# Performance work log

Hardware: AMD Instinct MI355X
Metric: run time of the kernel (lower is better)

Reference implementation:

```python
import jax, jax.numpy as jnp
import numpy as np

TEMPERATURE = 0.1  # init kwarg
EPS = 1e-8        # torch cosine_similarity eps


def setup_inputs() -> dict:
    key = jax.random.key(0)
    k1, k2, k3 = jax.random.split(key, 3)
    B, D, C = 4096, 1024, 32
    representations = jax.random.normal(k1, (B, D), dtype=jnp.float32)
    soft_labels = jax.random.uniform(k2, (B, C), dtype=jnp.float32)
    labels = jax.random.randint(k3, (B,), 0, 32, dtype=jnp.int64)
    return {
        "representations": representations,
        "soft_labels": soft_labels,
        "labels": labels,
        "pseudo_weight": 10,
    }


def reference(representations, soft_labels, labels, pseudo_weight):
    B = representations.shape[0]
    # row-normalize (cosine similarity)
    norms = jnp.maximum(jnp.linalg.norm(representations, axis=1, keepdims=True), EPS)
    rn = representations / norms
    Z = (rn @ rn.T) / TEMPERATURE                      # [B, B] scaled cosine sims
    E = jnp.exp(Z)
    off_diag = 1.0 - jnp.eye(B, dtype=Z.dtype)         # exclude j == i
    denom = jnp.sum(E * off_diag, axis=1, keepdims=True)   # [B, 1]
    loss_arr = -(Z - jnp.log(denom))                   # -log(exp(Z_ij)/denom_i)
    # positive-pair weights: same label, j != i (detached in original)
    pos = (labels[:, None] == labels[None, :]).astype(Z.dtype) * off_diag
    soft_sim = jax.lax.stop_gradient(soft_labels @ soft_labels.T)  # torch.inner, detached
    w = pos + pseudo_weight * soft_sim
    return jnp.sum(loss_arr * w) / B
```

## Files before the change

kernel.cpp:

```cpp
#include <hip/hip_runtime.h>
#include <hip/hip_bf16.h>
#include <stdint.h>


typedef float f32x4 __attribute__((ext_vector_type(4)));
typedef long i64;

#define INV_T 10.0f
#define Z_SCALE (INV_T / 256.0f)

#define GLD16(gp, lp)                                                          \
    __builtin_amdgcn_global_load_lds(                                          \
        (const __attribute__((address_space(1))) uint32_t*)(gp),               \
        (__attribute__((address_space(3))) uint32_t*)(lp), 16, 0, 0)

#define OFF_RNF8  0
#define OFF_DENOM 4194304
#define OFF_POSS  (OFF_DENOM + 16384)
#define OFF_G     (OFF_POSS + 16384)
#define OFF_CSUM  (OFF_G + 131072)
#define OFF_CCNT  (OFF_CSUM + 128)
#define OFF_OACC  (OFF_CCNT + 128)
#define OFF_DONE  (OFF_OACC + 16)
#define WS_END    (OFF_DONE + 16)
#define ZERO_BYTES (WS_END - OFF_DENOM)

__global__ __launch_bounds__(256) void scl_norm_prep(const float* __restrict__ rep,
                                                     const float* __restrict__ sl,
                                                     const int* __restrict__ labels,
                                                     uint32_t* __restrict__ rnf8,
                                                     float* __restrict__ csum,
                                                     int* __restrict__ ccnt) {
    int b = blockIdx.x;
    int t = threadIdx.x;
    if (b < 4096) {
        int row = b;
        const float4* src = reinterpret_cast<const float4*>(rep + (size_t)row * 1024);
        float4 v = src[t];
        float s = v.x * v.x + v.y * v.y + v.z * v.z + v.w * v.w;
#pragma unroll
        for (int m = 1; m < 64; m <<= 1) s += __shfl_xor(s, m, 64);
        __shared__ float red[4];
        if ((t & 63) == 0) red[t >> 6] = s;
        __syncthreads();
        s = red[0] + red[1] + red[2] + red[3];
        float nf = 16.0f / fmaxf(sqrtf(s), 1e-8f);
        int p = 0;
        p = __builtin_amdgcn_cvt_pk_fp8_f32(v.x * nf, v.y * nf, p, false);
        p = __builtin_amdgcn_cvt_pk_fp8_f32(v.z * nf, v.w * nf, p, true);
        rnf8[row * 256 + t] = (uint32_t)p;
    } else {
        __shared__ float part[8][32];
        __shared__ int bins[32];
        int bb = b - 4096;
        if (t < 32) bins[t] = 0;
        __syncthreads();
        if (t < 128) atomicAdd(&bins[labels[bb * 128 + t]], 1);
        int c = t & 31, rg = t >> 5;
        float s = 0.f;
#pragma unroll 4
        for (int k = 0; k < 16; ++k) {
            int i = bb * 128 + rg * 16 + k;
            s += sl[i * 32 + c];
        }
        part[rg][c] = s;
        __syncthreads();
        if (t < 32) {
            float tot = 0.f;
#pragma unroll
            for (int g = 0; g < 8; ++g) tot += part[g][t];
            atomicAdd(&csum[t], tot);
            atomicAdd(&ccnt[t], bins[t]);
        }
    }
}

__global__ __launch_bounds__(256) void scl_G(const uint8_t* __restrict__ rnf8,
                                             const float* __restrict__ sl,
                                             float* __restrict__ G) {
    int t = threadIdx.x;
    int dblk = blockIdx.x & 15, ks = blockIdx.x >> 4;
    int dq = t >> 5, c = t & 31;
    int d0 = dblk * 64 + dq * 8;
    float acc[8];
#pragma unroll
    for (int j = 0; j < 8; ++j) acc[j] = 0.f;
    int i0 = ks * 128;
#pragma unroll 4
    for (int k = 0; k < 128; ++k) {
        int i = i0 + k;
        uint2 rv = *(const uint2*)&rnf8[(size_t)i * 1024 + d0];
        float sv = sl[i * 32 + c];
        acc[0] += __builtin_amdgcn_cvt_f32_fp8((int)rv.x, 0) * sv;
        acc[1] += __builtin_amdgcn_cvt_f32_fp8((int)rv.x, 1) * sv;
        acc[2] += __builtin_amdgcn_cvt_f32_fp8((int)rv.x, 2) * sv;
        acc[3] += __builtin_amdgcn_cvt_f32_fp8((int)rv.x, 3) * sv;
        acc[4] += __builtin_amdgcn_cvt_f32_fp8((int)rv.y, 0) * sv;
        acc[5] += __builtin_amdgcn_cvt_f32_fp8((int)rv.y, 1) * sv;
        acc[6] += __builtin_amdgcn_cvt_f32_fp8((int)rv.y, 2) * sv;
        acc[7] += __builtin_amdgcn_cvt_f32_fp8((int)rv.y, 3) * sv;
    }
#pragma unroll
    for (int j = 0; j < 8; ++j)
        atomicAdd(&G[(d0 + j) * 32 + c], acc[j] * 0.0625f);
}

__global__ __launch_bounds__(256) void scl_gemm(const uint8_t* __restrict__ rnf8,
                                                const int* __restrict__ labels,
                                                float* __restrict__ denom,
                                                float* __restrict__ posS) {
    __shared__ __align__(16) uint8_t As[128 * 64];
    __shared__ __align__(16) uint8_t Bs[128 * 64];
    __shared__ int lblA[128], lblB[128];

    int L = blockIdx.x;
    int bi = 0, rem = L;
    while (rem >= 32 - bi) { rem -= 32 - bi; ++bi; }
    int bj = bi + rem;
    int rowA0 = bi * 128, colB0 = bj * 128;

    int tid = threadIdx.x;
    if (tid < 128) {
        lblA[tid] = labels[rowA0 + tid];
        lblB[tid] = labels[colB0 + tid];
    }

    int lane = tid & 63, warp = tid >> 6;
    int wr = warp >> 1, wc = warp & 1;
    int m_ = lane & 15, g = lane >> 4;

    int r4 = lane >> 2;
    int csw = (lane & 3) ^ ((lane >> 3) & 3);
    const uint8_t* gA0 = rnf8 + (size_t)(rowA0 + warp * 32 + r4) * 1024 + csw * 16;
    const uint8_t* gB0 = rnf8 + (size_t)(colB0 + warp * 32 + r4) * 1024 + csw * 16;

    f32x4 acc[4][4];
#pragma unroll
    for (int a = 0; a < 4; ++a)
#pragma unroll
        for (int b = 0; b < 4; ++b) acc[a][b] = (f32x4){0.f, 0.f, 0.f, 0.f};

    for (int kt = 0; kt < 16; ++kt) {
        __syncthreads();
        GLD16(gA0 + kt * 64,          &As[(warp * 32) * 64]);
        GLD16(gA0 + kt * 64 + 16384,  &As[(warp * 32 + 16) * 64]);
        GLD16(gB0 + kt * 64,          &Bs[(warp * 32) * 64]);
        GLD16(gB0 + kt * 64 + 16384,  &Bs[(warp * 32 + 16) * 64]);
        __syncthreads();
#pragma unroll
        for (int s = 0; s < 2; ++s) {
            i64 af[4], bf[4];
#pragma unroll
            for (int ti = 0; ti < 4; ++ti) {
                int rowLoc = wr * 64 + ti * 16 + m_;
                af[ti] = *(const i64*)&As[rowLoc * 64 + (((s * 4 + g) ^ (m_ & 6)) * 8)];
            }
#pragma unroll
            for (int tj = 0; tj < 4; ++tj) {
                int colLoc = wc * 64 + tj * 16 + m_;
                bf[tj] = *(const i64*)&Bs[colLoc * 64 + (((s * 4 + g) ^ (m_ & 6)) * 8)];
            }
#pragma unroll
            for (int ti = 0; ti < 4; ++ti)
#pragma unroll
                for (int tj = 0; tj < 4; ++tj)
                    acc[ti][tj] = __builtin_amdgcn_mfma_f32_16x16x32_fp8_fp8(
                        af[ti], bf[tj], acc[ti][tj], 0, 0, 0);
        }
    }

    bool isDiag = (bi == bj);
    int cl = m_;
    float colE[4] = {0.f, 0.f, 0.f, 0.f}, colP[4] = {0.f, 0.f, 0.f, 0.f};
#pragma unroll
    for (int ti = 0; ti < 4; ++ti) {
        int rowLoc = wr * 64 + ti * 16 + g * 4;
        float rE[4] = {0.f, 0.f, 0.f, 0.f}, rP[4] = {0.f, 0.f, 0.f, 0.f};
        int lr[4];
#pragma unroll
        for (int r = 0; r < 4; ++r) lr[r] = lblA[rowLoc + r];
#pragma unroll
        for (int tj = 0; tj < 4; ++tj) {
            int colLoc = wc * 64 + tj * 16 + cl;
            int gCol = colB0 + colLoc;
            int lc = lblB[colLoc];
            f32x4 a = acc[ti][tj];
#pragma unroll
            for (int r = 0; r < 4; ++r) {
                int gRow = rowA0 + rowLoc + r;
                float z = Z_SCALE * a[r];
                float e = __expf(z);
                bool offd = (gRow != gCol);
                if (!offd) e = 0.f;
                rE[r] += e;
                colE[tj] += e;
                if (offd && (lr[r] == lc)) { rP[r] += z; colP[tj] += z; }
            }
        }
#pragma unroll
        for (int r = 0; r < 4; ++r) {
            float v = rE[r], p = rP[r];
#pragma unroll
            for (int msk = 1; msk < 16; msk <<= 1) {
                v += __shfl_xor(v, msk, 64);
                p += __shfl_xor(p, msk, 64);
            }
            if (cl == 0) {
                int gRow = rowA0 + rowLoc + r;
                atomicAdd(&denom[gRow], v);
                atomicAdd(&posS[gRow], p);
            }
        }
    }
    if (!isDiag) {
#pragma unroll
        for (int tj = 0; tj < 4; ++tj) {
            float v = colE[tj], p = colP[tj];
            v += __shfl_xor(v, 16, 64); p += __shfl_xor(p, 16, 64);
            v += __shfl_xor(v, 32, 64); p += __shfl_xor(p, 32, 64);
            if (g == 0) {
                int gCol = colB0 + wc * 64 + tj * 16 + cl;
                atomicAdd(&denom[gCol], v);
                atomicAdd(&posS[gCol], p);
            }
        }
    }
}

__global__ __launch_bounds__(256) void scl_finalize(const float* __restrict__ denom,
                                                    const float* __restrict__ posS,
                                                    const float* __restrict__ sl,
                                                    const int* __restrict__ labels,
                                                    const int* __restrict__ ccnt,
                                                    const float* __restrict__ csum,
                                                    const float* __restrict__ G,
                                                    const int* __restrict__ pwp,
                                                    double* __restrict__ oacc,
                                                    int* __restrict__ done,
                                                    float* __restrict__ out) {
    int t = threadIdx.x;
    int bits = *pwp;
    float pw = (bits >= -(1 << 22) && bits <= (1 << 22)) ? (float)bits : __int_as_float(bits);
    __shared__ double wsum[4];
    double contrib = 0.0;

    if (blockIdx.x < 16) {
        int i = blockIdx.x * 256 + t;
        const f32x4* sl4 = (const f32x4*)sl;
        const f32x4* cs4 = (const f32x4*)csum;
        float dW = 0.f;
#pragma unroll
        for (int q = 0; q < 8; ++q) {
            f32x4 s = sl4[i * 8 + q];
            f32x4 c = cs4[q];
            dW += s[0] * c[0] + s[1] * c[1] + s[2] * c[2] + s[3] * c[3];
        }
        float W = (float)(ccnt[labels[i]] - 1) + pw * dW;
        float term = __logf(denom[i]) * W - posS[i];
        double td = (double)term;
#pragma unroll
        for (int m = 1; m < 64; m <<= 1) td += __shfl_xor(td, m, 64);
        if ((t & 63) == 0) wsum[t >> 6] = td;
        __syncthreads();
        contrib = wsum[0] + wsum[1] + wsum[2] + wsum[3];
    } else {
        const f32x4* G4 = (const f32x4*)G;
        float gs = 0.f;
#pragma unroll
        for (int q = 0; q < 32; ++q) {
            f32x4 v = G4[q * 256 + t];
            gs += v[0] * v[0] + v[1] * v[1] + v[2] * v[2] + v[3] * v[3];
        }
        double gd = (double)gs;
#pragma unroll
        for (int m = 1; m < 64; m <<= 1) gd += __shfl_xor(gd, m, 64);
        if ((t & 63) == 0) wsum[t >> 6] = gd;
        __syncthreads();
        contrib = -(double)(pw * INV_T) * (wsum[0] + wsum[1] + wsum[2] + wsum[3]);
    }

    if (t == 0) {
        atomicAdd(oacc, contrib);
        __threadfence();
        int old = atomicAdd(done, 1);
        if (old == 16) {
            double tot = atomicAdd(oacc, 0.0);
            out[0] = (float)(tot * (1.0 / 4096.0));
        }
    }
}

extern "C" void kernel_launch(void* const* d_in, const int* in_sizes, int n_in,
                              void* d_out, int out_size, void* d_ws, size_t ws_size,
                              hipStream_t stream) {
    const float* rep = (const float*)d_in[0];
    const float* sl = (const float*)d_in[1];
    const int* labels = (const int*)d_in[2];
    const int* pwp = (const int*)d_in[3];

    char* ws = (char*)d_ws;
    uint8_t* rnf8 = (uint8_t*)(ws + OFF_RNF8);
    float* denom = (float*)(ws + OFF_DENOM);
    float* posS = (float*)(ws + OFF_POSS);
    float* G = (float*)(ws + OFF_G);
    float* csum = (float*)(ws + OFF_CSUM);
    int* ccnt = (int*)(ws + OFF_CCNT);
    double* oacc = (double*)(ws + OFF_OACC);
    int* done = (int*)(ws + OFF_DONE);

    hipMemsetAsync(ws + OFF_DENOM, 0, ZERO_BYTES, stream);

    scl_norm_prep<<<4128, 256, 0, stream>>>(rep, sl, labels, (uint32_t*)rnf8, csum, ccnt);
    scl_G<<<512, 256, 0, stream>>>(rnf8, sl, G);
    scl_gemm<<<528, 256, 0, stream>>>(rnf8, labels, denom, posS);
    scl_finalize<<<17, 256, 0, stream>>>(denom, posS, sl, labels, ccnt, csum, G, pwp,
                                         oacc, done, (float*)d_out);
}
```

Measured before the change: 132.7 us.

## Fold memset, G and weight computation into fewer kernel launches

Replaces the hipMemsetAsync with extra zeroing blocks in the first kernel. The class-sum atomics become per-block partial writes. The G kernel and a new per-row weight computation are merged into the GEMM launch as extra blocks, and finalize shrinks accordingly. The GEMM inner loop now loads 16-byte fragments once per k-tile, in place of two 8-byte loads per sub-step, using a new swizzle. These changes aim to cut launch and serialization overhead and LDS read instructions, at the cost of more heterogeneous blocks sharing one launch.

```diff
diff --git a/kernel.cpp b/kernel.cpp
--- a/kernel.cpp
+++ b/kernel.cpp
@@ -18,19 +18,20 @@
 #define OFF_DENOM 4194304
 #define OFF_POSS  (OFF_DENOM + 16384)
 #define OFF_G     (OFF_POSS + 16384)
-#define OFF_CSUM  (OFF_G + 131072)
-#define OFF_CCNT  (OFF_CSUM + 128)
-#define OFF_OACC  (OFF_CCNT + 128)
+#define OFF_OACC  (OFF_G + 131072)
 #define OFF_DONE  (OFF_OACC + 16)
-#define WS_END    (OFF_DONE + 16)
-#define ZERO_BYTES (WS_END - OFF_DENOM)
-
-__global__ __launch_bounds__(256) void scl_norm_prep(const float* __restrict__ rep,
-                                                     const float* __restrict__ sl,
-                                                     const int* __restrict__ labels,
-                                                     uint32_t* __restrict__ rnf8,
-                                                     float* __restrict__ csum,
-                                                     int* __restrict__ ccnt) {
+#define ZERO_SPAN 167936
+#define OFF_CSP   (OFF_DENOM + ZERO_SPAN)
+#define OFF_CCP   (OFF_CSP + 4096)
+#define OFF_W     (OFF_CCP + 4096)
+
+__global__ __launch_bounds__(256) void scl_stage1(const float* __restrict__ rep,
+                                                  const float* __restrict__ sl,
+                                                  const int* __restrict__ labels,
+                                                  uint32_t* __restrict__ rnf8,
+                                                  float* __restrict__ cs_part,
+                                                  int* __restrict__ cc_part,
+                                                  char* __restrict__ zbase) {
     int b = blockIdx.x;
     int t = threadIdx.x;
     if (b < 4096) {
@@ -49,7 +50,7 @@
         p = __builtin_amdgcn_cvt_pk_fp8_f32(v.x * nf, v.y * nf, p, false);
         p = __builtin_amdgcn_cvt_pk_fp8_f32(v.z * nf, v.w * nf, p, true);
         rnf8[row * 256 + t] = (uint32_t)p;
-    } else {
+    } else if (b < 4128) {
         __shared__ float part[8][32];
         __shared__ int bins[32];
         int bb = b - 4096;
@@ -69,46 +70,82 @@
             float tot = 0.f;
 #pragma unroll
             for (int g = 0; g < 8; ++g) tot += part[g][t];
-            atomicAdd(&csum[t], tot);
-            atomicAdd(&ccnt[t], bins[t]);
-        }
+            cs_part[bb * 32 + t] = tot;
+            cc_part[bb * 32 + t] = bins[t];
+        }
+    } else {
+        int zb = b - 4128;
+        *(uint4*)(zbase + (size_t)zb * 4096 + t * 16) = (uint4){0, 0, 0, 0};
     }
 }
 
-__global__ __launch_bounds__(256) void scl_G(const uint8_t* __restrict__ rnf8,
-                                             const float* __restrict__ sl,
-                                             float* __restrict__ G) {
-    int t = threadIdx.x;
-    int dblk = blockIdx.x & 15, ks = blockIdx.x >> 4;
-    int dq = t >> 5, c = t & 31;
-    int d0 = dblk * 64 + dq * 8;
-    float acc[8];
-#pragma unroll
-    for (int j = 0; j < 8; ++j) acc[j] = 0.f;
-    int i0 = ks * 128;
+__global__ __launch_bounds__(256) void scl_main(const uint8_t* __restrict__ rnf8,
+                                                const float* __restrict__ sl,
+                                                const int* __restrict__ labels,
+                                                const float* __restrict__ cs_part,
+                                                const int* __restrict__ cc_part,
+                                                const int* __restrict__ pwp,
+                                                float* __restrict__ denom,
+                                                float* __restrict__ posS,
+                                                float* __restrict__ G,
+                                                float* __restrict__ W) {
+    int tid = threadIdx.x;
+
+    if (blockIdx.x >= 528) {
+        if (blockIdx.x < 1040) {
+            int idx = blockIdx.x - 528;
+            int dblk = idx & 15, ks = idx >> 4;
+            int dq = tid >> 5, c = tid & 31;
+            int d0 = dblk * 64 + dq * 8;
+            float acc[8];
+#pragma unroll
+            for (int j = 0; j < 8; ++j) acc[j] = 0.f;
+            int i0 = ks * 128;
 #pragma unroll 4
-    for (int k = 0; k < 128; ++k) {
-        int i = i0 + k;
-        uint2 rv = *(const uint2*)&rnf8[(size_t)i * 1024 + d0];
-        float sv = sl[i * 32 + c];
-        acc[0] += __builtin_amdgcn_cvt_f32_fp8((int)rv.x, 0) * sv;
-        acc[1] += __builtin_amdgcn_cvt_f32_fp8((int)rv.x, 1) * sv;
-        acc[2] += __builtin_amdgcn_cvt_f32_fp8((int)rv.x, 2) * sv;
-        acc[3] += __builtin_amdgcn_cvt_f32_fp8((int)rv.x, 3) * sv;
-        acc[4] += __builtin_amdgcn_cvt_f32_fp8((int)rv.y, 0) * sv;
-        acc[5] += __builtin_amdgcn_cvt_f32_fp8((int)rv.y, 1) * sv;
-        acc[6] += __builtin_amdgcn_cvt_f32_fp8((int)rv.y, 2) * sv;
-        acc[7] += __builtin_amdgcn_cvt_f32_fp8((int)rv.y, 3) * sv;
-    }
-#pragma unroll
-    for (int j = 0; j < 8; ++j)
-        atomicAdd(&G[(d0 + j) * 32 + c], acc[j] * 0.0625f);
-}
-
-__global__ __launch_bounds__(256) void scl_gemm(const uint8_t* __restrict__ rnf8,
-                                                const int* __restrict__ labels,
-                                                float* __restrict__ denom,
-                                                float* __restrict__ posS) {
+            for (int k = 0; k < 128; ++k) {
+                int i = i0 + k;
+                uint2 rv = *(const uint2*)&rnf8[(size_t)i * 1024 + d0];
+                float sv = sl[i * 32 + c];
+                acc[0] += __builtin_amdgcn_cvt_f32_fp8((int)rv.x, 0) * sv;
+                acc[1] += __builtin_amdgcn_cvt_f32_fp8((int)rv.x, 1) * sv;
+                acc[2] += __builtin_amdgcn_cvt_f32_fp8((int)rv.x, 2) * sv;
+                acc[3] += __builtin_amdgcn_cvt_f32_fp8((int)rv.x, 3) * sv;
+                acc[4] += __builtin_amdgcn_cvt_f32_fp8((int)rv.y, 0) * sv;
+                acc[5] += __builtin_amdgcn_cvt_f32_fp8((int)rv.y, 1) * sv;
+                acc[6] += __builtin_amdgcn_cvt_f32_fp8((int)rv.y, 2) * sv;
+                acc[7] += __builtin_amdgcn_cvt_f32_fp8((int)rv.y, 3) * sv;
+            }
+#pragma unroll
+            for (int j = 0; j < 8; ++j)
+                atomicAdd(&G[(d0 + j) * 32 + c], acc[j] * 0.0625f);
+        } else {
+            __shared__ __align__(16) float css[32];
+            __shared__ int ccs[32];
+            if (tid < 32) {
+                float s = 0.f; int n = 0;
+#pragma unroll
+                for (int b = 0; b < 32; ++b) { s += cs_part[b * 32 + tid]; n += cc_part[b * 32 + tid]; }
+                css[tid] = s; ccs[tid] = n;
+            }
+            __syncthreads();
+            int bits = *pwp;
+            float pw = (bits >= -(1 << 22) && bits <= (1 << 22)) ? (float)bits
+                                                                 : __int_as_float(bits);
+            int i = (blockIdx.x - 1040) * 256 + tid;
+            const f32x4* sl4 = (const f32x4*)sl;
+            const f32x4* cs4 = (const f32x4*)css;
+            float dW = 0.f;
+#pragma unroll
+            for (int q = 0; q < 8; ++q) {
+                f32x4 s = sl4[i * 8 + q];
+                f32x4 c = cs4[q];
+                dW += s[0] * c[0] + s[1] * c[1] + s[2] * c[2] + s[3] * c[3];
+            }
+            W[i] = (float)(ccs[labels[i]] - 1) + pw * dW;
+        }
+        return;
+    }
+
     __shared__ __align__(16) uint8_t As[128 * 64];
     __shared__ __align__(16) uint8_t Bs[128 * 64];
     __shared__ int lblA[128], lblB[128];
@@ -119,7 +156,6 @@
     int bj = bi + rem;
     int rowA0 = bi * 128, colB0 = bj * 128;
 
-    int tid = threadIdx.x;
     if (tid < 128) {
         lblA[tid] = labels[rowA0 + tid];
         lblB[tid] = labels[colB0 + tid];
@@ -140,33 +176,37 @@
 #pragma unroll
         for (int b = 0; b < 4; ++b) acc[a][b] = (f32x4){0.f, 0.f, 0.f, 0.f};
 
+    int fsw = (g ^ ((m_ >> 1) & 3)) * 16;
+
     for (int kt = 0; kt < 16; ++kt) {
         __syncthreads();
-        GLD16(gA0 + kt * 64,          &As[(warp * 32) * 64]);
-        GLD16(gA0 + kt * 64 + 16384,  &As[(warp * 32 + 16) * 64]);
-        GLD16(gB0 + kt * 64,          &Bs[(warp * 32) * 64]);
-        GLD16(gB0 + kt * 64 + 16384,  &Bs[(warp * 32 + 16) * 64]);
-        __syncthreads();
-#pragma unroll
-        for (int s = 0; s < 2; ++s) {
-            i64 af[4], bf[4];
-#pragma unroll
-            for (int ti = 0; ti < 4; ++ti) {
-                int rowLoc = wr * 64 + ti * 16 + m_;
-                af[ti] = *(const i64*)&As[rowLoc * 64 + (((s * 4 + g) ^ (m_ & 6)) * 8)];
-            }
-#pragma unroll
-            for (int tj = 0; tj < 4; ++tj) {
-                int colLoc = wc * 64 + tj * 16 + m_;
-                bf[tj] = *(const i64*)&Bs[colLoc * 64 + (((s * 4 + g) ^ (m_ & 6)) * 8)];
-            }
+        GLD16(gA0 + kt * 64,         &As[(warp * 32) * 64]);
+        GLD16(gA0 + kt * 64 + 16384, &As[(warp * 32 + 16) * 64]);
+        GLD16(gB0 + kt * 64,         &Bs[(warp * 32) * 64]);
+        GLD16(gB0 + kt * 64 + 16384, &Bs[(warp * 32 + 16) * 64]);
+        __syncthreads();
+        f32x4 aq[4], bq[4];
+#pragma unroll
+        for (int ti = 0; ti < 4; ++ti) {
+            int rowLoc = wr * 64 + ti * 16 + m_;
+            aq[ti] = *(const f32x4*)&As[rowLoc * 64 + fsw];
+        }
+#pragma unroll
+        for (int tj = 0; tj < 4; ++tj) {
+            int colLoc = wc * 64 + tj * 16 + m_;
+            bq[tj] = *(const f32x4*)&Bs[colLoc * 64 + fsw];
+        }
+#pragma unroll
+        for (int s = 0; s < 2; ++s)
 #pragma unroll
             for (int ti = 0; ti < 4; ++ti)
 #pragma unroll
-                for (int tj = 0; tj < 4; ++tj)
+                for (int tj = 0; tj < 4; ++tj) {
+                    i64 a = ((const i64*)&aq[ti])[s];
+                    i64 b = ((const i64*)&bq[tj])[s];
                     acc[ti][tj] = __builtin_amdgcn_mfma_f32_16x16x32_fp8_fp8(
-                        af[ti], bf[tj], acc[ti][tj], 0, 0, 0);
-        }
+                        a, b, acc[ti][tj], 0, 0, 0);
+                }
     }
 
     bool isDiag = (bi == bj);
@@ -229,41 +269,30 @@
 
 __global__ __launch_bounds__(256) void scl_finalize(const float* __restrict__ denom,
                                                     const float* __restrict__ posS,
-                                                    const float* __restrict__ sl,
-                                                    const int* __restrict__ labels,
-                                                    const int* __restrict__ ccnt,
-                                                    const float* __restrict__ csum,
+                                                    const float* __restrict__ W,
                                                     const float* __restrict__ G,
                                                     const int* __restrict__ pwp,
                                                     double* __restrict__ oacc,
                                                     int* __restrict__ done,
                                                     float* __restrict__ out) {
     int t = threadIdx.x;
-    int bits = *pwp;
-    float pw = (bits >= -(1 << 22) && bits <= (1 << 22)) ? (float)bits : __int_as_float(bits);
     __shared__ double wsum[4];
     double contrib = 0.0;
 
-    if (blockIdx.x < 16) {
-        int i = blockIdx.x * 256 + t;
-        const f32x4* sl4 = (const f32x4*)sl;
-        const f32x4* cs4 = (const f32x4*)csum;
-        float dW = 0.f;
-#pragma unroll
-        for (int q = 0; q < 8; ++q) {
-            f32x4 s = sl4[i * 8 + q];
-            f32x4 c = cs4[q];
-            dW += s[0] * c[0] + s[1] * c[1] + s[2] * c[2] + s[3] * c[3];
-        }
-        float W = (float)(ccnt[labels[i]] - 1) + pw * dW;
-        float term = __logf(denom[i]) * W - posS[i];
-        double td = (double)term;
+    if (blockIdx.x < 8) {
+        int i0 = blockIdx.x * 512 + t;
+        float t0 = __logf(denom[i0]) * W[i0] - posS[i0];
+        float t1 = __logf(denom[i0 + 256]) * W[i0 + 256] - posS[i0 + 256];
+        double td = (double)t0 + (double)t1;
 #pragma unroll
         for (int m = 1; m < 64; m <<= 1) td += __shfl_xor(td, m, 64);
         if ((t & 63) == 0) wsum[t >> 6] = td;
         __syncthreads();
         contrib = wsum[0] + wsum[1] + wsum[2] + wsum[3];
     } else {
+        int bits = *pwp;
+        float pw = (bits >= -(1 << 22) && bits <= (1 << 22)) ? (float)bits
+                                                             : __int_as_float(bits);
         const f32x4* G4 = (const f32x4*)G;
         float gs = 0.f;
 #pragma unroll
@@ -283,7 +312,7 @@
         atomicAdd(oacc, contrib);
         __threadfence();
         int old = atomicAdd(done, 1);
-        if (old == 16) {
+        if (old == 8) {
             double tot = atomicAdd(oacc, 0.0);
             out[0] = (float)(tot * (1.0 / 4096.0));
         }
@@ -303,16 +332,16 @@
     float* denom = (float*)(ws + OFF_DENOM);
     float* posS = (float*)(ws + OFF_POSS);
     float* G = (float*)(ws + OFF_G);
-    float* csum = (float*)(ws + OFF_CSUM);
-    int* ccnt = (int*)(ws + OFF_CCNT);
     double* oacc = (double*)(ws + OFF_OACC);
     int* done = (int*)(ws + OFF_DONE);
-
-    hipMemsetAsync(ws + OFF_DENOM, 0, ZERO_BYTES, stream);
-
-    scl_norm_prep<<<4128, 256, 0, stream>>>(rep, sl, labels, (uint32_t*)rnf8, csum, ccnt);
-    scl_G<<<512, 256, 0, stream>>>(rnf8, sl, G);
-    scl_gemm<<<528, 256, 0, stream>>>(rnf8, labels, denom, posS);
-    scl_finalize<<<17, 256, 0, stream>>>(denom, posS, sl, labels, ccnt, csum, G, pwp,
-                                         oacc, done, (float*)d_out);
+    float* cs_part = (float*)(ws + OFF_CSP);
+    int* cc_part = (int*)(ws + OFF_CCP);
+    float* W = (float*)(ws + OFF_W);
+
+    scl_stage1<<<4169, 256, 0, stream>>>(rep, sl, labels, (uint32_t*)rnf8,
+                                         cs_part, cc_part, ws + OFF_DENOM);
+    scl_main<<<1056, 256, 0, stream>>>(rnf8, sl, labels, cs_part, cc_part, pwp,
+                                       denom, posS, G, W);
+    scl_finalize<<<9, 256, 0, stream>>>(denom, posS, W, G, pwp, oacc, done,
+                                        (float*)d_out);
 }
```

After: 118.3 us. 1.12x faster.
